# Kernel tuning notes

Hardware: AMD Instinct MI355X
Metric: run time of the kernel (lower is better)

The kernel has to match this reference:

```python
import jax, jax.numpy as jnp
import numpy as np

B, N, HS = 2, 2048, 1024
H, D = 16, 64
GRID = 16           # crop_size // patch_size
SEG = 20            # d_dim = h_dim = w_dim = 2*(64//3//2)


def setup_inputs() -> dict:
    key = jax.random.key(0)
    ks = jax.random.split(key, 5)
    s = 0.02
    return {
        "hidden_states": jax.random.normal(ks[0], (B, N, HS), jnp.float32),
        "Wq": jax.random.normal(ks[1], (HS, HS), jnp.float32) * s,
        "bq": jnp.zeros((HS,), jnp.float32),
        "Wk": jax.random.normal(ks[2], (HS, HS), jnp.float32) * s,
        "bk": jnp.zeros((HS,), jnp.float32),
        "Wv": jax.random.normal(ks[3], (HS, HS), jnp.float32) * s,
        "bv": jnp.zeros((HS,), jnp.float32),
        "Wp": jax.random.normal(ks[4], (HS, HS), jnp.float32) * s,
        "bp": jnp.zeros((HS,), jnp.float32),
    }


def _rope(x, pos):
    # x: [B, H, N, d], pos: [N] int. Faithful to rotate_queries_or_keys:
    # sin/cos are TILED (concat of two copies), rotation is pairwise interleaved.
    d = x.shape[-1]
    omega = 1.0 / (10000.0 ** (jnp.arange(d // 2, dtype=x.dtype) / (d / 2.0)))
    freq = pos.astype(x.dtype)[:, None] * omega          # [N, d/2]
    sin = jnp.tile(jnp.sin(freq), (1, 2))                # [N, d]
    cos = jnp.tile(jnp.cos(freq), (1, 2))
    xp = x.reshape(x.shape[:-1] + (d // 2, 2))
    rot = jnp.stack([-xp[..., 1], xp[..., 0]], axis=-1).reshape(x.shape)
    return x * cos + rot * sin


def _apply_rope3d(qk, fpos, hpos, wpos):
    parts, s = [], 0
    for pos in (fpos, hpos, wpos):
        parts.append(_rope(qk[..., s:s + SEG], pos))
        s += SEG
    parts.append(qk[..., s:])  # pass-through remainder (4 dims)
    return jnp.concatenate(parts, axis=-1)


def reference(hidden_states, Wq, bq, Wk, bk, Wv, bv, Wp, bp):
    b, n, _ = hidden_states.shape

    def heads(x):  # [B,N,HS] -> [B,H,N,D]
        return x.reshape(b, n, H, D).transpose(0, 2, 1, 3)

    q = heads(hidden_states @ Wq.T + bq)
    k = heads(hidden_states @ Wk.T + bk)
    v = heads(hidden_states @ Wv.T + bv)

    ids = jnp.arange(n)
    tpf = GRID * GRID
    fpos = ids // tpf
    rem = ids - fpos * tpf
    hpos = rem // GRID
    wpos = rem - hpos * GRID

    q = _apply_rope3d(q, fpos, hpos, wpos)
    k = _apply_rope3d(k, fpos, hpos, wpos)

    scores = jnp.einsum('bhqd,bhkd->bhqk', q, k) * (D ** -0.5)
    probs = jax.nn.softmax(scores.astype(jnp.float32), axis=-1).astype(q.dtype)
    ctx = jnp.einsum('bhqk,bhkd->bqhd', probs, v).reshape(b, n, HS)
    return ctx @ Wp.T + bp
```

## Files before the change

### kernel.cpp

```cpp
#include <hip/hip_runtime.h>
#include <hip/hip_bf16.h>
#include <math.h>

#define BB    2
#define NN    2048
#define HSZ   1024
#define NH    16
#define HD    64
#define SEGW  20

#define LOG2E  1.4426950408889634f
#define QSCALE (0.125f * LOG2E)
#define DTHR   8.0f

typedef unsigned short u16;
typedef unsigned int   u32;
using bf16x8 = __attribute__((ext_vector_type(8))) short;
using f32x4  = __attribute__((ext_vector_type(4))) float;
using f32x16 = __attribute__((ext_vector_type(16))) float;

__device__ __forceinline__ u16 f2b(float f) {
    union { float f; u32 u; } x; x.f = f;
    u32 r = x.u + 0x7FFF + ((x.u >> 16) & 1);
    return (u16)(r >> 16);
}
__device__ __forceinline__ u16 f2bc(float f) {
    __hip_bfloat16 h = __float2bfloat16(f);
    return *reinterpret_cast<u16*>(&h);
}

__device__ __forceinline__ void gload16(void* lds, const void* g) {
    __builtin_amdgcn_global_load_lds(
        (const __attribute__((address_space(1))) void*)g,
        (__attribute__((address_space(3))) void*)lds, 16, 0, 0);
}

__device__ __forceinline__ void pswap(u32& a, u32& b) {
    asm volatile("v_permlane32_swap_b32 %0, %1" : "+v"(a), "+v"(b));
}

__global__ __launch_bounds__(256)
void cast_k(const float* __restrict__ hs, const float* __restrict__ Wq,
            const float* __restrict__ Wk, const float* __restrict__ Wv,
            const float* __restrict__ Wp, u16* __restrict__ hsb,
            u16* __restrict__ wqb, u16* __restrict__ wkb,
            u16* __restrict__ wvb, u16* __restrict__ wpb) {
    size_t idx = ((size_t)blockIdx.x * 256 + threadIdx.x) * 4;
    const float* s; u16* d; size_t o;
    const size_t HSN = 4194304, WN = 1048576;
    if      (idx < HSN)          { s = hs; d = hsb; o = idx; }
    else if (idx < HSN + WN)     { s = Wq; d = wqb; o = idx - HSN; }
    else if (idx < HSN + 2*WN)   { s = Wk; d = wkb; o = idx - HSN - WN; }
    else if (idx < HSN + 3*WN)   { s = Wv; d = wvb; o = idx - HSN - 2*WN; }
    else                         { s = Wp; d = wpb; o = idx - HSN - 3*WN; }
    float4 v = *(const float4*)(s + o);
    u32 lo = f2b(v.x) | ((u32)f2b(v.y) << 16);
    u32 hi = f2b(v.z) | ((u32)f2b(v.w) << 16);
    *(uint2*)(d + o) = uint2{lo, hi};
}

__global__ void rope_table_k(float* __restrict__ tab) {
    int n = blockIdx.x, d = threadIdx.x;
    float c = 1.f, s = 0.f;
    if (d < 3 * SEGW) {
        int seg = d / SEGW;
        int jj  = (d % SEGW) % (SEGW / 2);
        int rem = n & 255;
        int pos = (seg == 0) ? (n >> 8) : ((seg == 1) ? (rem >> 4) : (rem & 15));
        float omega = powf(10000.f, -(float)jj / 10.f);
        float fr = (float)pos * omega;
        s = sinf(fr); c = cosf(fr);
    }
    tab[(n * 64 + d) * 2 + 0] = c;
    tab[(n * 64 + d) * 2 + 1] = s;
}

__device__ __forceinline__
void gemm_body(const u16* __restrict__ X, const u16* __restrict__ Wb,
               const float* __restrict__ bias, void* __restrict__ out,
               const float* __restrict__ tab, int mode) {
    __shared__ u16 As[2][128 * 32];
    __shared__ u16 Bs[2][128 * 32];

    const int t  = threadIdx.x;
    const int w  = t >> 6;
    const int l  = t & 63;
    const int flat = blockIdx.x + (blockIdx.y << 3);
    const int o0 = (flat >> 5) * 128;
    const int m0 = (flat & 31) * 128;
    const int wr = (w >> 1) * 64;
    const int wc = (w & 1) * 64;

    const int ch  = (w << 6) + l;
    const int rA0 = ch >> 2,         cA0 = (((ch & 3) ^ (rA0 & 3))) * 8;
    const int rA1 = (ch + 256) >> 2, cA1 = (((ch & 3) ^ (rA1 & 3))) * 8;
    const int kbyte = (((l >> 4) ^ (l & 3)) << 4);

    f32x4 acc[4][4] = {};

    gload16(As[0] + ((w << 6)) * 8,       X  + (size_t)(m0 + rA0) * HSZ + cA0);
    gload16(As[0] + (256 + (w << 6)) * 8, X  + (size_t)(m0 + rA1) * HSZ + cA1);
    gload16(Bs[0] + ((w << 6)) * 8,       Wb + (size_t)(o0 + rA0) * HSZ + cA0);
    gload16(Bs[0] + (256 + (w << 6)) * 8, Wb + (size_t)(o0 + rA1) * HSZ + cA1);
    __syncthreads();

    int cur = 0;
    for (int k0 = 0; k0 < HSZ; k0 += 32, cur ^= 1) {
        if (k0 + 32 < HSZ) {
            int kn = k0 + 32;
            gload16(As[cur ^ 1] + ((w << 6)) * 8,       X  + (size_t)(m0 + rA0) * HSZ + kn + cA0);
            gload16(As[cur ^ 1] + (256 + (w << 6)) * 8, X  + (size_t)(m0 + rA1) * HSZ + kn + cA1);
            gload16(Bs[cur ^ 1] + ((w << 6)) * 8,       Wb + (size_t)(o0 + rA0) * HSZ + kn + cA0);
            gload16(Bs[cur ^ 1] + (256 + (w << 6)) * 8, Wb + (size_t)(o0 + rA1) * HSZ + kn + cA1);
        }
        bf16x8 af[4], bfr[4];
#pragma unroll
        for (int i = 0; i < 4; ++i) {
            int row = wr + i * 16 + (l & 15);
            af[i] = *(const bf16x8*)((const char*)As[cur] + row * 64 + kbyte);
        }
#pragma unroll
        for (int j = 0; j < 4; ++j) {
            int row = wc + j * 16 + (l & 15);
            bfr[j] = *(const bf16x8*)((const char*)Bs[cur] + row * 64 + kbyte);
        }
        __builtin_amdgcn_s_setprio(1);
#pragma unroll
        for (int i = 0; i < 4; ++i)
#pragma unroll
            for (int j = 0; j < 4; ++j)
                acc[i][j] = __builtin_amdgcn_mfma_f32_16x16x32_bf16(af[i], bfr[j], acc[i][j], 0, 0, 0);
        __builtin_amdgcn_s_setprio(0);
        __syncthreads();
    }

#pragma unroll
    for (int j = 0; j < 4; ++j) {
        int oc = o0 + wc + j * 16 + (l & 15);
        int h  = oc >> 6;
        int d  = oc & 63;
        float bv = bias[oc];
        if (mode == 2) {
#pragma unroll
            for (int rt = 0; rt < 4; ++rt) {
                int base = m0 + wr + rt * 16 + (l >> 4) * 4;
                int b_ = base >> 11, n0 = base & (NN - 1);
                u16 e[4];
#pragma unroll
                for (int r = 0; r < 4; ++r) e[r] = f2b(acc[rt][j][r] + bv);
                u32 lo = e[0] | ((u32)e[1] << 16);
                u32 hi = e[2] | ((u32)e[3] << 16);
                u16* vp = (u16*)out + (((size_t)b_ * NH + h) * HD + d) * NN + n0;
                *(uint2*)vp = uint2{lo, hi};
            }
        } else if (mode == 3) {
#pragma unroll
            for (int rt = 0; rt < 4; ++rt)
#pragma unroll
                for (int r = 0; r < 4; ++r) {
                    int m = m0 + wr + rt * 16 + (l >> 4) * 4 + r;
                    ((float*)out)[(size_t)m * HSZ + oc] = acc[rt][j][r] + bv;
                }
        } else {
            float scl = (mode == 0) ? QSCALE : 1.f;
#pragma unroll
            for (int rt = 0; rt < 4; ++rt)
#pragma unroll
                for (int r = 0; r < 4; ++r) {
                    int m = m0 + wr + rt * 16 + (l >> 4) * 4 + r;
                    int n = m & (NN - 1), b_ = m >> 11;
                    float v = acc[rt][j][r] + bv;
                    float2 cs = ((const float2*)tab)[n * 64 + d];
                    float part = __shfl_xor(v, 1);
                    float vr = (l & 1) ? fmaf(part, cs.y, v * cs.x)
                                       : fmaf(-part, cs.y, v * cs.x);
                    u16* qp = (u16*)out + (((size_t)b_ * NH + h) * NN + n) * HD + d;
                    *qp = f2b(vr * scl);
                }
        }
    }
}

__global__ __launch_bounds__(256)
void qkv_k(const u16* __restrict__ X,
           const u16* __restrict__ Wq, const u16* __restrict__ Wk, const u16* __restrict__ Wv,
           const float* __restrict__ bq, const float* __restrict__ bk, const float* __restrict__ bv,
           u16* __restrict__ qo, u16* __restrict__ ko, u16* __restrict__ vo,
           const float* __restrict__ tab) {
    int z = blockIdx.z;
    const u16* W   = (z == 0) ? Wq : (z == 1) ? Wk : Wv;
    const float* b = (z == 0) ? bq : (z == 1) ? bk : bv;
    u16* o         = (z == 0) ? qo : (z == 1) ? ko : vo;
    gemm_body(X, W, b, o, tab, z);
}

__global__ __launch_bounds__(256)
void projo_k(const u16* __restrict__ X, const u16* __restrict__ W,
             const float* __restrict__ b, float* __restrict__ out) {
    gemm_body(X, W, b, out, nullptr, 3);
}

__global__ __launch_bounds__(256)
void attn_mfma_k(const u16* __restrict__ Qb, const u16* __restrict__ Kb,
                 const u16* __restrict__ Vtb, u16* __restrict__ ctxb) {
    __shared__ u16 KVs[2][2][64 * 64];

    const int t = threadIdx.x, w = t >> 6, l = t & 63;
    const int h = l >> 5;
    int f  = blockIdx.y * 16 + blockIdx.x;
    int bh = (f & 7) * 4 + ((f >> 3) & 3);
    int qt = f >> 5;
    const int b_ = bh >> 4, hd = bh & 15;

    const u16* Qg = Qb + ((size_t)bh * NN + qt * 128) * HD;
    const u16* Kg = Kb + (size_t)bh * NN * HD;
    const u16* Vg = Vtb + (size_t)bh * HD * NN;

    const int xr   = (l & 7) << 4;
    const int h16  = h * 16;
    const int rowo = (l & 31) * 128;
    int kb4[4];
#pragma unroll
    for (int ks = 0; ks < 4; ++ks) kb4[ks] = ((ks * 32) | h16) ^ xr;

    const int ch  = w * 64 + l;
    const int r0  = ch >> 3,          sl0 = (ch & 7) ^ (r0 & 7);
    const int r1  = (ch + 256) >> 3,  sl1 = (ch & 7) ^ (r1 & 7);

#pragma unroll
    for (int s = 0; s < 4; ++s) {
        int c = s * 256 + ch;
        int row = c >> 3, sl = (c & 7) ^ (row & 7);
        gload16(&KVs[0][0][0] + (s * 256 + w * 64) * 8, Qg + row * HD + sl * 8);
    }
    __syncthreads();
    bf16x8 qf[4];
    {
        const char* Ql = (const char*)&KVs[0][0][0];
        int qrow = (w * 32 + (l & 31)) * 128;
#pragma unroll
        for (int ks = 0; ks < 4; ++ks)
            qf[ks] = *(const bf16x8*)(Ql + qrow + kb4[ks]);
    }
    __syncthreads();

    gload16(&KVs[0][0][0] + (w * 64) * 8,        Kg + (size_t)r0 * HD + sl0 * 8);
    gload16(&KVs[0][0][0] + (256 + w * 64) * 8,  Kg + (size_t)r1 * HD + sl1 * 8);
    gload16(&KVs[0][1][0] + (w * 64) * 8,        Vg + (size_t)r0 * NN + sl0 * 8);
    gload16(&KVs[0][1][0] + (256 + w * 64) * 8,  Vg + (size_t)r1 * NN + sl1 * 8);
    __syncthreads();

    float m_i = -INFINITY, l_i = 0.f;
    f32x16 oa0 = {}, oa1 = {};

    int cur = 0;
    for (int kt = 0; kt < NN / 64; ++kt, cur ^= 1) {
        if (kt + 1 < NN / 64) {
            int nx = (kt + 1) * 64;
            gload16(&KVs[cur ^ 1][0][0] + (w * 64) * 8,       Kg + (size_t)(nx + r0) * HD + sl0 * 8);
            gload16(&KVs[cur ^ 1][0][0] + (256 + w * 64) * 8, Kg + (size_t)(nx + r1) * HD + sl1 * 8);
            gload16(&KVs[cur ^ 1][1][0] + (w * 64) * 8,       Vg + (size_t)r0 * NN + nx + sl0 * 8);
            gload16(&KVs[cur ^ 1][1][0] + (256 + w * 64) * 8, Vg + (size_t)r1 * NN + nx + sl1 * 8);
        }

        const char* Kl = (const char*)&KVs[cur][0][0];
        f32x16 sa0 = {}, sa1 = {};
        __builtin_amdgcn_s_setprio(1);
#pragma unroll
        for (int ks = 0; ks < 4; ++ks) {
            bf16x8 k0 = *(const bf16x8*)(Kl + rowo + kb4[ks]);
            bf16x8 k1 = *(const bf16x8*)(Kl + 4096 + rowo + kb4[ks]);
            sa0 = __builtin_amdgcn_mfma_f32_32x32x16_bf16(k0, qf[ks], sa0, 0, 0, 0);
            sa1 = __builtin_amdgcn_mfma_f32_32x32x16_bf16(k1, qf[ks], sa1, 0, 0, 0);
        }
        __builtin_amdgcn_s_setprio(0);

        float mx8[8];
#pragma unroll
        for (int j = 0; j < 8; ++j)
            mx8[j] = fmaxf(fmaxf(sa0[j], sa0[j + 8]), fmaxf(sa1[j], sa1[j + 8]));
        float pm = fmaxf(fmaxf(fmaxf(mx8[0], mx8[1]), fmaxf(mx8[2], mx8[3])),
                         fmaxf(fmaxf(mx8[4], mx8[5]), fmaxf(mx8[6], mx8[7])));
        if (__any(pm > m_i + DTHR)) {
            float mx = fmaxf(pm, __shfl_xor(pm, 32));
            float mn = fmaxf(m_i, mx);
            float alpha = __builtin_amdgcn_exp2f(m_i - mn);
            m_i = mn;
            l_i *= alpha;
#pragma unroll
            for (int r = 0; r < 16; ++r) { oa0[r] *= alpha; oa1[r] *= alpha; }
        }

        u32 o_[16];
        float ls0 = 0.f, ls1 = 0.f, ls2 = 0.f, ls3 = 0.f;
#pragma unroll
        for (int j = 0; j < 8; ++j) {
            float pa = __builtin_amdgcn_exp2f(sa0[2 * j]     - m_i);
            float pb = __builtin_amdgcn_exp2f(sa0[2 * j + 1] - m_i);
            float pc = __builtin_amdgcn_exp2f(sa1[2 * j]     - m_i);
            float pd = __builtin_amdgcn_exp2f(sa1[2 * j + 1] - m_i);
            ls0 += pa; ls1 += pb; ls2 += pc; ls3 += pd;
            o_[j]     = (u32)f2bc(pa) | ((u32)f2bc(pb) << 16);
            o_[8 + j] = (u32)f2bc(pc) | ((u32)f2bc(pd) << 16);
        }
        l_i += (ls0 + ls1) + (ls2 + ls3);

        pswap(o_[0], o_[2]);   pswap(o_[1], o_[3]);
        pswap(o_[4], o_[6]);   pswap(o_[5], o_[7]);
        pswap(o_[8], o_[10]);  pswap(o_[9], o_[11]);
        pswap(o_[12], o_[14]); pswap(o_[13], o_[15]);

        const char* Vl = (const char*)&KVs[cur][1][0];
        __builtin_amdgcn_s_setprio(1);
#pragma unroll
        for (int ks2 = 0; ks2 < 4; ++ks2) {
            union { u32 u[4]; bf16x8 v; } fr;
            fr.u[0] = o_[4 * ks2 + 0]; fr.u[1] = o_[4 * ks2 + 1];
            fr.u[2] = o_[4 * ks2 + 2]; fr.u[3] = o_[4 * ks2 + 3];
            bf16x8 v0 = *(const bf16x8*)(Vl + rowo + kb4[ks2]);
            bf16x8 v1 = *(const bf16x8*)(Vl + 4096 + rowo + kb4[ks2]);
            oa0 = __builtin_amdgcn_mfma_f32_32x32x16_bf16(v0, fr.v, oa0, 0, 0, 0);
            oa1 = __builtin_amdgcn_mfma_f32_32x32x16_bf16(v1, fr.v, oa1, 0, 0, 0);
        }
        __builtin_amdgcn_s_setprio(0);

        __syncthreads();
    }

    float lt = l_i + __shfl_xor(l_i, 32);
    float inv = 1.f / lt;
    int n = qt * 128 + w * 32 + (l & 31);
    u16* op = ctxb + ((size_t)b_ * NN + n) * HSZ + hd * 64;
#pragma unroll
    for (int dt = 0; dt < 2; ++dt) {
        const f32x16& oa = dt ? oa1 : oa0;
#pragma unroll
        for (int rg = 0; rg < 4; ++rg) {
            int d0 = 4 * h + 8 * rg + 32 * dt;
            u16 e0 = f2bc(oa[4 * rg + 0] * inv);
            u16 e1 = f2bc(oa[4 * rg + 1] * inv);
            u16 e2 = f2bc(oa[4 * rg + 2] * inv);
            u16 e3 = f2bc(oa[4 * rg + 3] * inv);
            *(uint2*)(op + d0) = uint2{e0 | ((u32)e1 << 16), e2 | ((u32)e3 << 16)};
        }
    }
}

extern "C" void kernel_launch(void* const* d_in, const int* in_sizes, int n_in,
                              void* d_out, int out_size, void* d_ws, size_t ws_size,
                              hipStream_t stream) {
    (void)in_sizes; (void)n_in; (void)out_size; (void)ws_size;
    const float* hs = (const float*)d_in[0];
    const float* Wq = (const float*)d_in[1];
    const float* bq = (const float*)d_in[2];
    const float* Wk = (const float*)d_in[3];
    const float* bk = (const float*)d_in[4];
    const float* Wv = (const float*)d_in[5];
    const float* bv = (const float*)d_in[6];
    const float* Wp = (const float*)d_in[7];
    const float* bp = (const float*)d_in[8];

    char* ws = (char*)d_ws;
    u16*   hsb  = (u16*)(ws);
    u16*   Wqb  = (u16*)(ws + 8388608);
    u16*   Wkb  = (u16*)(ws + 10485760);
    u16*   Wvb  = (u16*)(ws + 12582912);
    u16*   Wpb  = (u16*)(ws + 14680064);
    u16*   qb   = (u16*)(ws + 16777216);
    u16*   kb   = (u16*)(ws + 25165824);
    u16*   vtb  = (u16*)(ws + 33554432);
    u16*   ctxb = (u16*)(ws + 41943040);
    float* tab  = (float*)(ws + 50331648);

    cast_k<<<8192, 256, 0, stream>>>(hs, Wq, Wk, Wv, Wp, hsb, Wqb, Wkb, Wvb, Wpb);
    rope_table_k<<<NN, 64, 0, stream>>>(tab);

    qkv_k<<<dim3(HSZ / 128, (BB * NN) / 128, 3), 256, 0, stream>>>(
        hsb, Wqb, Wkb, Wvb, bq, bk, bv, qb, kb, vtb, tab);

    attn_mfma_k<<<dim3(NN / 128, BB * NH), 256, 0, stream>>>(qb, kb, vtb, ctxb);

    projo_k<<<dim3(HSZ / 128, (BB * NN) / 128), 256, 0, stream>>>(ctxb, Wpb, bp, (float*)d_out);
}
```

Before: 140.4 us.

## Fuse rope table into cast kernel, load GEMM weights directly, MFMA row sums

Merges the RoPE table generation into the cast kernel so one launch is saved. In the GEMM, the weight operand is now read straight from global memory into registers with a one-step prefetch, which halves LDS usage and removes the B-tile LDS reads. In attention, the softmax row sum is computed with an extra MFMA against a vector of ones, the max reduction uses v_max3, and P is packed with v_cvt_pk_bf16_f32. The trade-off is uncoalesced direct global weight loads, an extra MFMA per k-step, and accumulating the row sum from bf16-rounded probabilities.

```diff
diff --git a/kernel.cpp b/kernel.cpp
--- a/kernel.cpp
+++ b/kernel.cpp
@@ -28,6 +28,16 @@
     __hip_bfloat16 h = __float2bfloat16(f);
     return *reinterpret_cast<u16*>(&h);
 }
+__device__ __forceinline__ u32 cvtpk(float lo, float hi) {
+    u32 r;
+    asm("v_cvt_pk_bf16_f32 %0, %1, %2" : "=v"(r) : "v"(lo), "v"(hi));
+    return r;
+}
+__device__ __forceinline__ float max3(float a, float b, float c) {
+    float d;
+    asm("v_max3_f32 %0, %1, %2, %3" : "=v"(d) : "v"(a), "v"(b), "v"(c));
+    return d;
+}
 
 __device__ __forceinline__ void gload16(void* lds, const void* g) {
     __builtin_amdgcn_global_load_lds(
@@ -40,11 +50,29 @@
 }
 
 __global__ __launch_bounds__(256)
-void cast_k(const float* __restrict__ hs, const float* __restrict__ Wq,
-            const float* __restrict__ Wk, const float* __restrict__ Wv,
-            const float* __restrict__ Wp, u16* __restrict__ hsb,
-            u16* __restrict__ wqb, u16* __restrict__ wkb,
-            u16* __restrict__ wvb, u16* __restrict__ wpb) {
+void cast_rope_k(const float* __restrict__ hs, const float* __restrict__ Wq,
+                 const float* __restrict__ Wk, const float* __restrict__ Wv,
+                 const float* __restrict__ Wp, u16* __restrict__ hsb,
+                 u16* __restrict__ wqb, u16* __restrict__ wkb,
+                 u16* __restrict__ wvb, u16* __restrict__ wpb,
+                 float* __restrict__ tab) {
+    if (blockIdx.x >= 8192) {
+        int idx = (blockIdx.x - 8192) * 256 + threadIdx.x;
+        int n = idx >> 6, d = idx & 63;
+        float c = 1.f, s = 0.f;
+        if (d < 3 * SEGW) {
+            int seg = d / SEGW;
+            int jj  = (d % SEGW) % (SEGW / 2);
+            int rem = n & 255;
+            int pos = (seg == 0) ? (n >> 8) : ((seg == 1) ? (rem >> 4) : (rem & 15));
+            float omega = powf(10000.f, -(float)jj / 10.f);
+            float fr = (float)pos * omega;
+            s = sinf(fr); c = cosf(fr);
+        }
+        tab[idx * 2 + 0] = c;
+        tab[idx * 2 + 1] = s;
+        return;
+    }
     size_t idx = ((size_t)blockIdx.x * 256 + threadIdx.x) * 4;
     const float* s; u16* d; size_t o;
     const size_t HSN = 4194304, WN = 1048576;
@@ -59,28 +87,11 @@
     *(uint2*)(d + o) = uint2{lo, hi};
 }
 
-__global__ void rope_table_k(float* __restrict__ tab) {
-    int n = blockIdx.x, d = threadIdx.x;
-    float c = 1.f, s = 0.f;
-    if (d < 3 * SEGW) {
-        int seg = d / SEGW;
-        int jj  = (d % SEGW) % (SEGW / 2);
-        int rem = n & 255;
-        int pos = (seg == 0) ? (n >> 8) : ((seg == 1) ? (rem >> 4) : (rem & 15));
-        float omega = powf(10000.f, -(float)jj / 10.f);
-        float fr = (float)pos * omega;
-        s = sinf(fr); c = cosf(fr);
-    }
-    tab[(n * 64 + d) * 2 + 0] = c;
-    tab[(n * 64 + d) * 2 + 1] = s;
-}
-
 __device__ __forceinline__
 void gemm_body(const u16* __restrict__ X, const u16* __restrict__ Wb,
                const float* __restrict__ bias, void* __restrict__ out,
                const float* __restrict__ tab, int mode) {
     __shared__ u16 As[2][128 * 32];
-    __shared__ u16 Bs[2][128 * 32];
 
     const int t  = threadIdx.x;
     const int w  = t >> 6;
@@ -96,41 +107,46 @@
     const int rA1 = (ch + 256) >> 2, cA1 = (((ch & 3) ^ (rA1 & 3))) * 8;
     const int kbyte = (((l >> 4) ^ (l & 3)) << 4);
 
+    const u16* bp[4];
+#pragma unroll
+    for (int j = 0; j < 4; ++j)
+        bp[j] = Wb + (size_t)(o0 + wc + j * 16 + (l & 15)) * HSZ + ((l >> 4) << 3);
+
     f32x4 acc[4][4] = {};
-
-    gload16(As[0] + ((w << 6)) * 8,       X  + (size_t)(m0 + rA0) * HSZ + cA0);
-    gload16(As[0] + (256 + (w << 6)) * 8, X  + (size_t)(m0 + rA1) * HSZ + cA1);
-    gload16(Bs[0] + ((w << 6)) * 8,       Wb + (size_t)(o0 + rA0) * HSZ + cA0);
-    gload16(Bs[0] + (256 + (w << 6)) * 8, Wb + (size_t)(o0 + rA1) * HSZ + cA1);
+    bf16x8 bc[4], bn[4];
+
+    gload16(As[0] + ((w << 6)) * 8,       X + (size_t)(m0 + rA0) * HSZ + cA0);
+    gload16(As[0] + (256 + (w << 6)) * 8, X + (size_t)(m0 + rA1) * HSZ + cA1);
+#pragma unroll
+    for (int j = 0; j < 4; ++j) bc[j] = *(const bf16x8*)(bp[j]);
     __syncthreads();
 
     int cur = 0;
     for (int k0 = 0; k0 < HSZ; k0 += 32, cur ^= 1) {
         if (k0 + 32 < HSZ) {
             int kn = k0 + 32;
-            gload16(As[cur ^ 1] + ((w << 6)) * 8,       X  + (size_t)(m0 + rA0) * HSZ + kn + cA0);
-            gload16(As[cur ^ 1] + (256 + (w << 6)) * 8, X  + (size_t)(m0 + rA1) * HSZ + kn + cA1);
-            gload16(Bs[cur ^ 1] + ((w << 6)) * 8,       Wb + (size_t)(o0 + rA0) * HSZ + kn + cA0);
-            gload16(Bs[cur ^ 1] + (256 + (w << 6)) * 8, Wb + (size_t)(o0 + rA1) * HSZ + kn + cA1);
-        }
-        bf16x8 af[4], bfr[4];
+            gload16(As[cur ^ 1] + ((w << 6)) * 8,       X + (size_t)(m0 + rA0) * HSZ + kn + cA0);
+            gload16(As[cur ^ 1] + (256 + (w << 6)) * 8, X + (size_t)(m0 + rA1) * HSZ + kn + cA1);
+#pragma unroll
+            for (int j = 0; j < 4; ++j) bn[j] = *(const bf16x8*)(bp[j] + kn);
+        }
+        bf16x8 af[4];
 #pragma unroll
         for (int i = 0; i < 4; ++i) {
             int row = wr + i * 16 + (l & 15);
             af[i] = *(const bf16x8*)((const char*)As[cur] + row * 64 + kbyte);
         }
-#pragma unroll
-        for (int j = 0; j < 4; ++j) {
-            int row = wc + j * 16 + (l & 15);
-            bfr[j] = *(const bf16x8*)((const char*)Bs[cur] + row * 64 + kbyte);
-        }
         __builtin_amdgcn_s_setprio(1);
 #pragma unroll
         for (int i = 0; i < 4; ++i)
 #pragma unroll
             for (int j = 0; j < 4; ++j)
-                acc[i][j] = __builtin_amdgcn_mfma_f32_16x16x32_bf16(af[i], bfr[j], acc[i][j], 0, 0, 0);
+                acc[i][j] = __builtin_amdgcn_mfma_f32_16x16x32_bf16(af[i], bc[j], acc[i][j], 0, 0, 0);
         __builtin_amdgcn_s_setprio(0);
+        if (k0 + 32 < HSZ) {
+#pragma unroll
+            for (int j = 0; j < 4; ++j) bc[j] = bn[j];
+        }
         __syncthreads();
     }
 
@@ -250,8 +266,12 @@
     gload16(&KVs[0][1][0] + (256 + w * 64) * 8,  Vg + (size_t)r1 * NN + sl1 * 8);
     __syncthreads();
 
-    float m_i = -INFINITY, l_i = 0.f;
-    f32x16 oa0 = {}, oa1 = {};
+    bf16x8 ones;
+#pragma unroll
+    for (int i = 0; i < 8; ++i) ones[i] = (short)0x3F80;
+
+    float m_i = -INFINITY;
+    f32x16 oa0 = {}, oa1 = {}, lacc = {};
 
     int cur = 0;
     for (int kt = 0; kt < NN / 64; ++kt, cur ^= 1) {
@@ -275,35 +295,43 @@
         }
         __builtin_amdgcn_s_setprio(0);
 
-        float mx8[8];
-#pragma unroll
-        for (int j = 0; j < 8; ++j)
-            mx8[j] = fmaxf(fmaxf(sa0[j], sa0[j + 8]), fmaxf(sa1[j], sa1[j + 8]));
-        float pm = fmaxf(fmaxf(fmaxf(mx8[0], mx8[1]), fmaxf(mx8[2], mx8[3])),
-                         fmaxf(fmaxf(mx8[4], mx8[5]), fmaxf(mx8[6], mx8[7])));
-        if (__any(pm > m_i + DTHR)) {
-            float mx = fmaxf(pm, __shfl_xor(pm, 32));
+        float a0 = max3(sa0[0], sa0[1], sa0[2]);
+        float a1 = max3(sa0[3], sa0[4], sa0[5]);
+        float a2 = max3(sa0[6], sa0[7], sa0[8]);
+        float a3 = max3(sa0[9], sa0[10], sa0[11]);
+        float a4 = max3(sa0[12], sa0[13], sa0[14]);
+        float a5 = max3(sa1[0], sa1[1], sa1[2]);
+        float a6 = max3(sa1[3], sa1[4], sa1[5]);
+        float a7 = max3(sa1[6], sa1[7], sa1[8]);
+        float a8 = max3(sa1[9], sa1[10], sa1[11]);
+        float a9 = max3(sa1[12], sa1[13], sa1[14]);
+        float aa = fmaxf(sa0[15], sa1[15]);
+        float b0 = max3(a0, a1, a2);
+        float b1 = max3(a3, a4, a5);
+        float b2 = max3(a6, a7, a8);
+        float b3 = max3(a9, aa, b0);
+        float pmv = max3(b1, b2, b3);
+        if (__any(pmv > m_i + DTHR)) {
+            float mx = fmaxf(pmv, __shfl_xor(pmv, 32));
             float mn = fmaxf(m_i, mx);
             float alpha = __builtin_amdgcn_exp2f(m_i - mn);
             m_i = mn;
-            l_i *= alpha;
-#pragma unroll
-            for (int r = 0; r < 16; ++r) { oa0[r] *= alpha; oa1[r] *= alpha; }
+#pragma unroll
+            for (int r = 0; r < 16; ++r) {
+                oa0[r] *= alpha; oa1[r] *= alpha; lacc[r] *= alpha;
+            }
         }
 
         u32 o_[16];
-        float ls0 = 0.f, ls1 = 0.f, ls2 = 0.f, ls3 = 0.f;
 #pragma unroll
         for (int j = 0; j < 8; ++j) {
             float pa = __builtin_amdgcn_exp2f(sa0[2 * j]     - m_i);
             float pb = __builtin_amdgcn_exp2f(sa0[2 * j + 1] - m_i);
             float pc = __builtin_amdgcn_exp2f(sa1[2 * j]     - m_i);
             float pd = __builtin_amdgcn_exp2f(sa1[2 * j + 1] - m_i);
-            ls0 += pa; ls1 += pb; ls2 += pc; ls3 += pd;
-            o_[j]     = (u32)f2bc(pa) | ((u32)f2bc(pb) << 16);
-            o_[8 + j] = (u32)f2bc(pc) | ((u32)f2bc(pd) << 16);
-        }
-        l_i += (ls0 + ls1) + (ls2 + ls3);
+            o_[j]     = cvtpk(pa, pb);
+            o_[8 + j] = cvtpk(pc, pd);
+        }
 
         pswap(o_[0], o_[2]);   pswap(o_[1], o_[3]);
         pswap(o_[4], o_[6]);   pswap(o_[5], o_[7]);
@@ -319,6 +347,7 @@
             fr.u[2] = o_[4 * ks2 + 2]; fr.u[3] = o_[4 * ks2 + 3];
             bf16x8 v0 = *(const bf16x8*)(Vl + rowo + kb4[ks2]);
             bf16x8 v1 = *(const bf16x8*)(Vl + 4096 + rowo + kb4[ks2]);
+            lacc = __builtin_amdgcn_mfma_f32_32x32x16_bf16(ones, fr.v, lacc, 0, 0, 0);
             oa0 = __builtin_amdgcn_mfma_f32_32x32x16_bf16(v0, fr.v, oa0, 0, 0, 0);
             oa1 = __builtin_amdgcn_mfma_f32_32x32x16_bf16(v1, fr.v, oa1, 0, 0, 0);
         }
@@ -327,8 +356,7 @@
         __syncthreads();
     }
 
-    float lt = l_i + __shfl_xor(l_i, 32);
-    float inv = 1.f / lt;
+    float inv = 1.f / lacc[0];
     int n = qt * 128 + w * 32 + (l & 31);
     u16* op = ctxb + ((size_t)b_ * NN + n) * HSZ + hd * 64;
 #pragma unroll
@@ -372,8 +400,8 @@
     u16*   ctxb = (u16*)(ws + 41943040);
     float* tab  = (float*)(ws + 50331648);
 
-    cast_k<<<8192, 256, 0, stream>>>(hs, Wq, Wk, Wv, Wp, hsb, Wqb, Wkb, Wvb, Wpb);
-    rope_table_k<<<NN, 64, 0, stream>>>(tab);
+    cast_rope_k<<<8704, 256, 0, stream>>>(hs, Wq, Wk, Wv, Wp,
+                                          hsb, Wqb, Wkb, Wvb, Wpb, tab);
 
     qkv_k<<<dim3(HSZ / 128, (BB * NN) / 128, 3), 256, 0, stream>>>(
         hsb, Wqb, Wkb, Wvb, bq, bk, bv, qb, kb, vtb, tab);
```

After: 154.5 us. +10.1%, slower.
